# Optimization experiments

Measured on AMD Instinct MI355X. Metric: run time of the kernel, lower is better.

Reference implementation:

```python
import jax, jax.numpy as jnp
import numpy as np

ALPHA = 0.2  # LeakyReLU negative slope


def setup_inputs() -> dict:
    key = jax.random.key(0)
    k1, k2, k3, k4 = jax.random.split(key, 4)
    N, E, F_IN, F_OUT = 100000, 1600000, 128, 32
    x = jax.random.normal(k1, (N, F_IN), dtype=jnp.float32)
    W = jax.random.normal(k2, (F_IN, F_OUT), dtype=jnp.float32) * 0.1
    a = jax.random.normal(k3, (2 * F_OUT, 1), dtype=jnp.float32) * 0.1
    edge_index = jax.random.randint(k4, (2, E), 0, N, dtype=jnp.int64)
    return {"x": x, "W": W, "a": a, "edge_index": edge_index}


def reference(x, W, a, edge_index):
    N = x.shape[0]
    F_OUT = W.shape[1]
    Wx = x @ W  # [N, F_OUT]
    src = edge_index[0]  # row indices (softmax groups)
    dst = edge_index[1]
    # e = leakyrelu([Wx_i || Wx_j] @ a); split a to avoid materializing the concat
    a_src = a[:F_OUT, 0]
    a_dst = a[F_OUT:, 0]
    e = (Wx @ a_src)[src] + (Wx @ a_dst)[dst]  # [E]
    e = jnp.where(e >= 0, e, ALPHA * e)
    # sparse softmax over rows (src)
    m = jax.ops.segment_max(e, src, num_segments=N)  # -inf for empty rows
    m = jnp.where(jnp.isinf(m), 0.0, m)
    exp_v = jnp.exp(e - m[src])
    s = jax.ops.segment_sum(exp_v, src, num_segments=N)
    s = jnp.where(s == 0, 1.0, s)
    att = exp_v / s[src]  # [E]
    # sparse matmul: h[i] = sum_j att[i,j] * Wx[j]
    h = jax.ops.segment_sum(att[:, None] * Wx[dst], src, num_segments=N)
    return jax.nn.elu(h)
```

## Files before the change

### kernel.cpp

```cpp
#include <hip/hip_runtime.h>
#include <hip/hip_bf16.h>
#include <math.h>

#define ALPHA 0.2f
#define F_IN 128
#define F_OUT 32
#define BSHIFT 7
#define BNODES 128
#define DSTBITS 17
#define CHUNK 8192
#define SLABCAP 3072
#define NBKMAX 800
#define MAXPER 6
#define CURSTRIDE 16

typedef __attribute__((ext_vector_type(8))) short short8;
typedef __attribute__((ext_vector_type(4))) float float4v;
typedef __attribute__((ext_vector_type(2))) float float2v;

__device__ __forceinline__ short f2bf(float f) {
    __hip_bfloat16 h = __float2bfloat16(f);
    return __builtin_bit_cast(short, h);
}
__device__ __forceinline__ float bf_lo(unsigned u) {
    return __uint_as_float(u << 16);
}
__device__ __forceinline__ float bf_hi(unsigned u) {
    return __uint_as_float(u & 0xFFFF0000u);
}

__global__ __launch_bounds__(512) void k_phaseA(
    const float* __restrict__ x, const float* __restrict__ W,
    const float* __restrict__ a, unsigned short* __restrict__ Wxh,
    float* __restrict__ s1, float* __restrict__ s2, int nTiles, int N, int nT1,
    const int* __restrict__ src, const int* __restrict__ dst,
    int* __restrict__ bcur, unsigned* __restrict__ packed, int E, int NBK)
{
    if ((int)blockIdx.x < nT1) {
        __shared__ short Wt[32 * 136];
        for (int i = threadIdx.x; i < F_IN * F_OUT; i += 512) {
            int k = i >> 5, n = i & 31;
            Wt[n * 136 + k] = f2bf(W[i]);
        }
        __syncthreads();

        int wave = threadIdx.x >> 6;
        int lane = threadIdx.x & 63;
        int tile = blockIdx.x * 8 + wave;
        if (tile >= nTiles) return;

        int m    = lane & 15;
        int quad = lane >> 4;
        int row  = tile * 16 + m;
        int rowc = row < N ? row : N - 1;

        short8 bf[2][4];
#pragma unroll
        for (int t = 0; t < 2; ++t)
#pragma unroll
            for (int s = 0; s < 4; ++s)
                bf[t][s] = *(const short8*)&Wt[(t * 16 + m) * 136 + s * 32 + quad * 8];

        float4v acc0 = {0.f, 0.f, 0.f, 0.f};
        float4v acc1 = {0.f, 0.f, 0.f, 0.f};
        const float* xr = x + (size_t)rowc * F_IN + quad * 8;
#pragma unroll
        for (int s = 0; s < 4; ++s) {
            float4 xa = *(const float4*)(xr + s * 32);
            float4 xb = *(const float4*)(xr + s * 32 + 4);
            short8 af;
            af[0] = f2bf(xa.x); af[1] = f2bf(xa.y); af[2] = f2bf(xa.z); af[3] = f2bf(xa.w);
            af[4] = f2bf(xb.x); af[5] = f2bf(xb.y); af[6] = f2bf(xb.z); af[7] = f2bf(xb.w);
            acc0 = __builtin_amdgcn_mfma_f32_16x16x32_bf16(af, bf[0][s], acc0, 0, 0, 0);
            acc1 = __builtin_amdgcn_mfma_f32_16x16x32_bf16(af, bf[1][s], acc1, 0, 0, 0);
        }

        int rbase = tile * 16 + quad * 4;
#pragma unroll
        for (int r = 0; r < 4; ++r) {
            if (rbase + r < N) {
                Wxh[(size_t)(rbase + r) * F_OUT + m]      = (unsigned short)f2bf(acc0[r]);
                Wxh[(size_t)(rbase + r) * F_OUT + m + 16] = (unsigned short)f2bf(acc1[r]);
            }
        }

        float a1c0 = a[m], a1c1 = a[m + 16];
        float a2c0 = a[F_OUT + m], a2c1 = a[F_OUT + m + 16];
#pragma unroll
        for (int r = 0; r < 4; ++r) {
            float v1 = acc0[r] * a1c0 + acc1[r] * a1c1;
            float v2 = acc0[r] * a2c0 + acc1[r] * a2c1;
#pragma unroll
            for (int off = 8; off >= 1; off >>= 1) {
                v1 += __shfl_xor(v1, off, 16);
                v2 += __shfl_xor(v2, off, 16);
            }
            if (m == 0 && rbase + r < N) {
                s1[rbase + r] = v1;
                s2[rbase + r] = v2;
            }
        }
    } else {
        __shared__ int hist[NBKMAX];
        __shared__ int cur[NBKMAX];
        int t = threadIdx.x;
        for (int i = t; i < NBK; i += 512) hist[i] = 0;
        __syncthreads();
        int e0 = ((int)blockIdx.x - nT1) * CHUNK;
        int sreg[16], dreg[16];
#pragma unroll
        for (int k = 0; k < 4; ++k) {
            int e = e0 + k * 2048 + t * 4;
            int4 s4, d4;
            if (e + 3 < E) {
                s4 = *(const int4*)&src[e];
                d4 = *(const int4*)&dst[e];
            } else {
                s4.x = (e + 0 < E) ? src[e + 0] : -1;
                s4.y = (e + 1 < E) ? src[e + 1] : -1;
                s4.z = (e + 2 < E) ? src[e + 2] : -1;
                s4.w = (e + 3 < E) ? src[e + 3] : -1;
                d4.x = (e + 0 < E) ? dst[e + 0] : 0;
                d4.y = (e + 1 < E) ? dst[e + 1] : 0;
                d4.z = (e + 2 < E) ? dst[e + 2] : 0;
                d4.w = (e + 3 < E) ? dst[e + 3] : 0;
            }
            sreg[k * 4 + 0] = s4.x; dreg[k * 4 + 0] = d4.x;
            sreg[k * 4 + 1] = s4.y; dreg[k * 4 + 1] = d4.y;
            sreg[k * 4 + 2] = s4.z; dreg[k * 4 + 2] = d4.z;
            sreg[k * 4 + 3] = s4.w; dreg[k * 4 + 3] = d4.w;
        }
#pragma unroll
        for (int k = 0; k < 16; ++k)
            if (sreg[k] >= 0) atomicAdd(&hist[sreg[k] >> BSHIFT], 1);
        __syncthreads();
        for (int i = t; i < NBK; i += 512)
            if (hist[i] > 0) cur[i] = atomicAdd(&bcur[i * CURSTRIDE], hist[i]);
        __syncthreads();
#pragma unroll
        for (int k = 0; k < 16; ++k) {
            if (sreg[k] >= 0) {
                int b = sreg[k] >> BSHIFT;
                int p = atomicAdd(&cur[b], 1);
                if (p < SLABCAP)
                    packed[(size_t)b * SLABCAP + p] =
                        ((unsigned)(sreg[k] & (BNODES - 1)) << DSTBITS) | (unsigned)dreg[k];
            }
        }
    }
}

__global__ __launch_bounds__(512) void k_bnode(
    const unsigned* __restrict__ packed, const int* __restrict__ bcur,
    const float* __restrict__ s1, const float* __restrict__ s2,
    const unsigned short* __restrict__ Wxh, float* __restrict__ out, int N)
{
    __shared__ unsigned sorted[SLABCAP];
    __shared__ int rpl[BNODES];
    __shared__ int degl[BNODES];
    __shared__ int cur[BNODES];
    __shared__ int histl[BNODES];
    __shared__ float s1l[BNODES];
    __shared__ float stageL[8][16][32];
    __shared__ float sumsL[8][16];

    int b = blockIdx.x;
    int t = threadIdx.x;
    int n0 = b << BSHIFT;
    int cnt = min(bcur[b * CURSTRIDE], SLABCAP);
    const unsigned* pb = packed + (size_t)b * SLABCAP;

    if (t < BNODES) {
        histl[t] = 0;
        int n = n0 + t;
        s1l[t] = (n < N) ? s1[n] : 0.f;
    }
    __syncthreads();

    unsigned ereg[MAXPER];
#pragma unroll
    for (int k = 0; k < MAXPER; ++k) {
        int j = k * 512 + t;
        ereg[k] = (j < cnt) ? pb[j] : 0xFFFFFFFFu;
    }
#pragma unroll
    for (int k = 0; k < MAXPER; ++k)
        if (ereg[k] != 0xFFFFFFFFu) atomicAdd(&histl[ereg[k] >> DSTBITS], 1);
    __syncthreads();

    if (t < 64) {
        int aLo = histl[t], aHi = histl[t + 64];
        int sLo = aLo, sHi = aHi;
#pragma unroll
        for (int off = 1; off < 64; off <<= 1) {
            int vLo = __shfl_up(sLo, off, 64);
            int vHi = __shfl_up(sHi, off, 64);
            if (t >= off) { sLo += vLo; sHi += vHi; }
        }
        sHi += __shfl(sLo, 63, 64);
        rpl[t]      = sLo - aLo;  cur[t]      = sLo - aLo;  degl[t]      = aLo;
        rpl[t + 64] = sHi - aHi;  cur[t + 64] = sHi - aHi;  degl[t + 64] = aHi;
    }
    __syncthreads();

#pragma unroll
    for (int k = 0; k < MAXPER; ++k) {
        if (ereg[k] != 0xFFFFFFFFu) {
            int ls = ereg[k] >> DSTBITS;
            int p = atomicAdd(&cur[ls], 1);
            sorted[p] = ereg[k];
        }
    }
    __syncthreads();

    int g   = t >> 4;
    int l4  = t & 15;
    int es  = l4 >> 2;
    int fq  = l4 & 3;
    unsigned fqo = (unsigned)(fq << 4);
    int w    = t >> 6;
    int widx0 = (g & 3) << 2;

    for (int ni = 0; ni < 4; ++ni) {
        int ls = (g << 2) + ni;
        int n = n0 + ls;
        if (n >= N) break;
        int base = rpl[ls];
        int deg  = degl[ls];
        float s1n = s1l[ls];

        float2v acc01 = {0.f, 0.f};
        float2v acc23 = {0.f, 0.f};
        float2v acc45 = {0.f, 0.f};
        float2v acc67 = {0.f, 0.f};
        float sum = 0.f;

        for (int j0 = 0; j0 < deg; j0 += 16) {
            int j = j0 + l4;
            unsigned off_l = 0;
            float p_l = 0.f;
            if (j < deg) {
                int d_l = (int)(sorted[base + j] & ((1u << DSTBITS) - 1));
                off_l = (unsigned)d_l << 6;
                float ev = s1n + s2[d_l];
                ev = fmaxf(ev, ALPHA * ev);
                p_l = __expf(ev);
            }
            sum += p_l;
            int cnt2 = min(16, deg - j0);
            int nIter = (cnt2 + 3) >> 2;
            for (int it = 0; it < nIter; ++it) {
                int e = (it << 2) + es;
                float    p   = __shfl(p_l, e, 16);
                unsigned off = (unsigned)__shfl((int)off_l, e, 16);
                uint4 wv = *(const uint4*)((const char*)Wxh + (off | fqo));
                float2v pp = {p, p};
                acc01 += pp * (float2v){bf_lo(wv.x), bf_hi(wv.x)};
                acc23 += pp * (float2v){bf_lo(wv.y), bf_hi(wv.y)};
                acc45 += pp * (float2v){bf_lo(wv.z), bf_hi(wv.z)};
                acc67 += pp * (float2v){bf_lo(wv.w), bf_hi(wv.w)};
            }
        }
        float a0 = acc01.x, a1 = acc01.y, a2 = acc23.x, a3 = acc23.y;
        float a4 = acc45.x, a5 = acc45.y, a6 = acc67.x, a7 = acc67.y;
#pragma unroll
        for (int off = 4; off <= 8; off <<= 1) {
            a0 += __shfl_xor(a0, off, 16);
            a1 += __shfl_xor(a1, off, 16);
            a2 += __shfl_xor(a2, off, 16);
            a3 += __shfl_xor(a3, off, 16);
            a4 += __shfl_xor(a4, off, 16);
            a5 += __shfl_xor(a5, off, 16);
            a6 += __shfl_xor(a6, off, 16);
            a7 += __shfl_xor(a7, off, 16);
        }
#pragma unroll
        for (int off = 8; off >= 1; off >>= 1)
            sum += __shfl_xor(sum, off, 16);

        if (l4 < 4) {
            float4 v0; v0.x = a0; v0.y = a1; v0.z = a2; v0.w = a3;
            float4 v1; v1.x = a4; v1.y = a5; v1.z = a6; v1.w = a7;
            *(float4*)&stageL[w][widx0 + ni][l4 * 8]     = v0;
            *(float4*)&stageL[w][widx0 + ni][l4 * 8 + 4] = v1;
        }
        if (l4 == 0)
            sumsL[w][widx0 + ni] = sum;
    }

    {
        int lw = t & 63;
        int ln = lw >> 2;
        int fo = (lw & 3) * 8;
        int n = n0 + (w << 4) + ln;
        if (n < N) {
            float s = sumsL[w][ln];
            float inv = (s > 0.f) ? __builtin_amdgcn_rcpf(s) : 0.f;
            const float* sp = &stageL[w][ln][fo];
            float4 h0 = *(const float4*)sp;
            float4 h1 = *(const float4*)(sp + 4);
            h0.x *= inv; h0.y *= inv; h0.z *= inv; h0.w *= inv;
            h1.x *= inv; h1.y *= inv; h1.z *= inv; h1.w *= inv;
            h0.x = h0.x > 0.f ? h0.x : __expf(h0.x) - 1.f;
            h0.y = h0.y > 0.f ? h0.y : __expf(h0.y) - 1.f;
            h0.z = h0.z > 0.f ? h0.z : __expf(h0.z) - 1.f;
            h0.w = h0.w > 0.f ? h0.w : __expf(h0.w) - 1.f;
            h1.x = h1.x > 0.f ? h1.x : __expf(h1.x) - 1.f;
            h1.y = h1.y > 0.f ? h1.y : __expf(h1.y) - 1.f;
            h1.z = h1.z > 0.f ? h1.z : __expf(h1.z) - 1.f;
            h1.w = h1.w > 0.f ? h1.w : __expf(h1.w) - 1.f;
            float* op = &out[(size_t)n * F_OUT + fo];
            *(float4*)op       = h0;
            *(float4*)(op + 4) = h1;
        }
    }
}

extern "C" void kernel_launch(void* const* d_in, const int* in_sizes, int n_in,
                              void* d_out, int out_size, void* d_ws, size_t ws_size,
                              hipStream_t stream)
{
    const float* x = (const float*)d_in[0];
    const float* W = (const float*)d_in[1];
    const float* a = (const float*)d_in[2];
    const int*  ei = (const int*)d_in[3];

    int N = in_sizes[0] / F_IN;
    int E = in_sizes[3] / 2;
    const int* src = ei;
    const int* dst = ei + E;
    int NBK = (N + BNODES - 1) >> BSHIFT;
    int nTiles = (N + 15) / 16;
    int nT1 = (nTiles + 7) / 8;
    int nEB = (E + CHUNK - 1) / CHUNK;

    unsigned short* Wxh = (unsigned short*)d_ws;
    float*    s1       = (float*)d_ws + (size_t)16 * N;
    float*    s2       = s1 + N;
    int*      bcur     = (int*)(s2 + N);
    unsigned* packed   = (unsigned*)(bcur + NBKMAX * CURSTRIDE);

    float* out = (float*)d_out;

    hipMemsetAsync(bcur, 0, (size_t)NBKMAX * CURSTRIDE * 4, stream);

    k_phaseA<<<nT1 + nEB, 512, 0, stream>>>(x, W, a, Wxh, s1, s2, nTiles, N, nT1,
                                            src, dst, bcur, packed, E, NBK);
    k_bnode<<<NBK, 512, 0, stream>>>(packed, bcur, s1, s2, Wxh, out, N);
}
```

Measured before the change: 146.6 us.

## Double edge chunk per block, reload src in scatter pass, rotate bucket reservations

The edge-bucketing blocks now handle 16384 edges each instead of 8192. Instead of holding src/dst in registers, they stream src twice: once for the histogram and once with dst for the scatter. Global bucket-cursor reservations start at a per-block rotated offset to spread atomic contention across buckets. The GEMM branch now issues all x loads before the MFMA loop. These changes halve the number of bucketing blocks and their global atomics, at the cost of re-reading src and holding fewer edges in flight per thread.

```diff
diff --git a/kernel.cpp b/kernel.cpp
--- a/kernel.cpp
+++ b/kernel.cpp
@@ -8,7 +8,7 @@
 #define BSHIFT 7
 #define BNODES 128
 #define DSTBITS 17
-#define CHUNK 8192
+#define CHUNK 16384
 #define SLABCAP 3072
 #define NBKMAX 800
 #define MAXPER 6
@@ -61,16 +61,21 @@
             for (int s = 0; s < 4; ++s)
                 bf[t][s] = *(const short8*)&Wt[(t * 16 + m) * 136 + s * 32 + quad * 8];
 
+        const float* xr = x + (size_t)rowc * F_IN + quad * 8;
+        float4 xa[4], xb[4];
+#pragma unroll
+        for (int s = 0; s < 4; ++s) {
+            xa[s] = *(const float4*)(xr + s * 32);
+            xb[s] = *(const float4*)(xr + s * 32 + 4);
+        }
+
         float4v acc0 = {0.f, 0.f, 0.f, 0.f};
         float4v acc1 = {0.f, 0.f, 0.f, 0.f};
-        const float* xr = x + (size_t)rowc * F_IN + quad * 8;
 #pragma unroll
         for (int s = 0; s < 4; ++s) {
-            float4 xa = *(const float4*)(xr + s * 32);
-            float4 xb = *(const float4*)(xr + s * 32 + 4);
             short8 af;
-            af[0] = f2bf(xa.x); af[1] = f2bf(xa.y); af[2] = f2bf(xa.z); af[3] = f2bf(xa.w);
-            af[4] = f2bf(xb.x); af[5] = f2bf(xb.y); af[6] = f2bf(xb.z); af[7] = f2bf(xb.w);
+            af[0] = f2bf(xa[s].x); af[1] = f2bf(xa[s].y); af[2] = f2bf(xa[s].z); af[3] = f2bf(xa[s].w);
+            af[4] = f2bf(xb[s].x); af[5] = f2bf(xb[s].y); af[6] = f2bf(xb[s].z); af[7] = f2bf(xb[s].w);
             acc0 = __builtin_amdgcn_mfma_f32_16x16x32_bf16(af, bf[0][s], acc0, 0, 0, 0);
             acc1 = __builtin_amdgcn_mfma_f32_16x16x32_bf16(af, bf[1][s], acc1, 0, 0, 0);
         }
@@ -107,9 +112,35 @@
         for (int i = t; i < NBK; i += 512) hist[i] = 0;
         __syncthreads();
         int e0 = ((int)blockIdx.x - nT1) * CHUNK;
-        int sreg[16], dreg[16];
-#pragma unroll
-        for (int k = 0; k < 4; ++k) {
+
+#pragma unroll 2
+        for (int k = 0; k < 8; ++k) {
+            int e = e0 + k * 2048 + t * 4;
+            int4 s4;
+            if (e + 3 < E) {
+                s4 = *(const int4*)&src[e];
+            } else {
+                s4.x = (e + 0 < E) ? src[e + 0] : -1;
+                s4.y = (e + 1 < E) ? src[e + 1] : -1;
+                s4.z = (e + 2 < E) ? src[e + 2] : -1;
+                s4.w = (e + 3 < E) ? src[e + 3] : -1;
+            }
+            if (s4.x >= 0) atomicAdd(&hist[s4.x >> BSHIFT], 1);
+            if (s4.y >= 0) atomicAdd(&hist[s4.y >> BSHIFT], 1);
+            if (s4.z >= 0) atomicAdd(&hist[s4.z >> BSHIFT], 1);
+            if (s4.w >= 0) atomicAdd(&hist[s4.w >> BSHIFT], 1);
+        }
+        __syncthreads();
+
+        int rot = (((int)blockIdx.x - nT1) * 131) % NBK;
+        for (int j = t; j < NBK; j += 512) {
+            int i = j + rot; if (i >= NBK) i -= NBK;
+            if (hist[i] > 0) cur[i] = atomicAdd(&bcur[i * CURSTRIDE], hist[i]);
+        }
+        __syncthreads();
+
+#pragma unroll 2
+        for (int k = 0; k < 8; ++k) {
             int e = e0 + k * 2048 + t * 4;
             int4 s4, d4;
             if (e + 3 < E) {
@@ -125,26 +156,17 @@
                 d4.z = (e + 2 < E) ? dst[e + 2] : 0;
                 d4.w = (e + 3 < E) ? dst[e + 3] : 0;
             }
-            sreg[k * 4 + 0] = s4.x; dreg[k * 4 + 0] = d4.x;
-            sreg[k * 4 + 1] = s4.y; dreg[k * 4 + 1] = d4.y;
-            sreg[k * 4 + 2] = s4.z; dreg[k * 4 + 2] = d4.z;
-            sreg[k * 4 + 3] = s4.w; dreg[k * 4 + 3] = d4.w;
-        }
-#pragma unroll
-        for (int k = 0; k < 16; ++k)
-            if (sreg[k] >= 0) atomicAdd(&hist[sreg[k] >> BSHIFT], 1);
-        __syncthreads();
-        for (int i = t; i < NBK; i += 512)
-            if (hist[i] > 0) cur[i] = atomicAdd(&bcur[i * CURSTRIDE], hist[i]);
-        __syncthreads();
-#pragma unroll
-        for (int k = 0; k < 16; ++k) {
-            if (sreg[k] >= 0) {
-                int b = sreg[k] >> BSHIFT;
-                int p = atomicAdd(&cur[b], 1);
-                if (p < SLABCAP)
-                    packed[(size_t)b * SLABCAP + p] =
-                        ((unsigned)(sreg[k] & (BNODES - 1)) << DSTBITS) | (unsigned)dreg[k];
+            int sreg[4] = {s4.x, s4.y, s4.z, s4.w};
+            int dreg[4] = {d4.x, d4.y, d4.z, d4.w};
+#pragma unroll
+            for (int c = 0; c < 4; ++c) {
+                if (sreg[c] >= 0) {
+                    int b = sreg[c] >> BSHIFT;
+                    int p = atomicAdd(&cur[b], 1);
+                    if (p < SLABCAP)
+                        packed[(size_t)b * SLABCAP + p] =
+                            ((unsigned)(sreg[c] & (BNODES - 1)) << DSTBITS) | (unsigned)dreg[c];
+                }
             }
         }
     }
```

New measurement: 157.0 us. 1.07x slower.

## Store Wx in fp32 instead of bf16 and hoist x loads before MFMA

Applied to the files above, without the earlier changes.

Wx is now kept as fp32 in the workspace rather than bf16, so the gather in the aggregation kernel reads 32 bytes per lane with two float4 loads and skips the bf16 unpacking. This doubles the gathered Wx footprint and the random-gather traffic. It also issues all x row loads ahead of the MFMA loop to overlap their latency. The precision change removes bf16 rounding error on Wx at the cost of extra memory bandwidth.

```diff
diff --git a/kernel.cpp b/kernel.cpp
--- a/kernel.cpp
+++ b/kernel.cpp
@@ -22,16 +22,10 @@
     __hip_bfloat16 h = __float2bfloat16(f);
     return __builtin_bit_cast(short, h);
 }
-__device__ __forceinline__ float bf_lo(unsigned u) {
-    return __uint_as_float(u << 16);
-}
-__device__ __forceinline__ float bf_hi(unsigned u) {
-    return __uint_as_float(u & 0xFFFF0000u);
-}
 
 __global__ __launch_bounds__(512) void k_phaseA(
     const float* __restrict__ x, const float* __restrict__ W,
-    const float* __restrict__ a, unsigned short* __restrict__ Wxh,
+    const float* __restrict__ a, float* __restrict__ Wxh,
     float* __restrict__ s1, float* __restrict__ s2, int nTiles, int N, int nT1,
     const int* __restrict__ src, const int* __restrict__ dst,
     int* __restrict__ bcur, unsigned* __restrict__ packed, int E, int NBK)
@@ -61,16 +55,21 @@
             for (int s = 0; s < 4; ++s)
                 bf[t][s] = *(const short8*)&Wt[(t * 16 + m) * 136 + s * 32 + quad * 8];
 
+        const float* xr = x + (size_t)rowc * F_IN + quad * 8;
+        float4 xa[4], xb[4];
+#pragma unroll
+        for (int s = 0; s < 4; ++s) {
+            xa[s] = *(const float4*)(xr + s * 32);
+            xb[s] = *(const float4*)(xr + s * 32 + 4);
+        }
+
         float4v acc0 = {0.f, 0.f, 0.f, 0.f};
         float4v acc1 = {0.f, 0.f, 0.f, 0.f};
-        const float* xr = x + (size_t)rowc * F_IN + quad * 8;
 #pragma unroll
         for (int s = 0; s < 4; ++s) {
-            float4 xa = *(const float4*)(xr + s * 32);
-            float4 xb = *(const float4*)(xr + s * 32 + 4);
             short8 af;
-            af[0] = f2bf(xa.x); af[1] = f2bf(xa.y); af[2] = f2bf(xa.z); af[3] = f2bf(xa.w);
-            af[4] = f2bf(xb.x); af[5] = f2bf(xb.y); af[6] = f2bf(xb.z); af[7] = f2bf(xb.w);
+            af[0] = f2bf(xa[s].x); af[1] = f2bf(xa[s].y); af[2] = f2bf(xa[s].z); af[3] = f2bf(xa[s].w);
+            af[4] = f2bf(xb[s].x); af[5] = f2bf(xb[s].y); af[6] = f2bf(xb[s].z); af[7] = f2bf(xb[s].w);
             acc0 = __builtin_amdgcn_mfma_f32_16x16x32_bf16(af, bf[0][s], acc0, 0, 0, 0);
             acc1 = __builtin_amdgcn_mfma_f32_16x16x32_bf16(af, bf[1][s], acc1, 0, 0, 0);
         }
@@ -79,8 +78,8 @@
 #pragma unroll
         for (int r = 0; r < 4; ++r) {
             if (rbase + r < N) {
-                Wxh[(size_t)(rbase + r) * F_OUT + m]      = (unsigned short)f2bf(acc0[r]);
-                Wxh[(size_t)(rbase + r) * F_OUT + m + 16] = (unsigned short)f2bf(acc1[r]);
+                Wxh[(size_t)(rbase + r) * F_OUT + m]      = acc0[r];
+                Wxh[(size_t)(rbase + r) * F_OUT + m + 16] = acc1[r];
             }
         }
 
@@ -153,7 +152,7 @@
 __global__ __launch_bounds__(512) void k_bnode(
     const unsigned* __restrict__ packed, const int* __restrict__ bcur,
     const float* __restrict__ s1, const float* __restrict__ s2,
-    const unsigned short* __restrict__ Wxh, float* __restrict__ out, int N)
+    const float* __restrict__ Wxh, float* __restrict__ out, int N)
 {
     __shared__ unsigned sorted[SLABCAP];
     __shared__ int rpl[BNODES];
@@ -217,7 +216,7 @@
     int l4  = t & 15;
     int es  = l4 >> 2;
     int fq  = l4 & 3;
-    unsigned fqo = (unsigned)(fq << 4);
+    unsigned fqo = (unsigned)(fq << 5);
     int w    = t >> 6;
     int widx0 = (g & 3) << 2;
 
@@ -241,7 +240,7 @@
             float p_l = 0.f;
             if (j < deg) {
                 int d_l = (int)(sorted[base + j] & ((1u << DSTBITS) - 1));
-                off_l = (unsigned)d_l << 6;
+                off_l = (unsigned)d_l << 7;
                 float ev = s1n + s2[d_l];
                 ev = fmaxf(ev, ALPHA * ev);
                 p_l = __expf(ev);
@@ -253,12 +252,14 @@
                 int e = (it << 2) + es;
                 float    p   = __shfl(p_l, e, 16);
                 unsigned off = (unsigned)__shfl((int)off_l, e, 16);
-                uint4 wv = *(const uint4*)((const char*)Wxh + (off | fqo));
+                const char* wp = (const char*)Wxh + (off | fqo);
+                float4 w0 = *(const float4*)wp;
+                float4 w1 = *(const float4*)(wp + 16);
                 float2v pp = {p, p};
-                acc01 += pp * (float2v){bf_lo(wv.x), bf_hi(wv.x)};
-                acc23 += pp * (float2v){bf_lo(wv.y), bf_hi(wv.y)};
-                acc45 += pp * (float2v){bf_lo(wv.z), bf_hi(wv.z)};
-                acc67 += pp * (float2v){bf_lo(wv.w), bf_hi(wv.w)};
+                acc01 += pp * (float2v){w0.x, w0.y};
+                acc23 += pp * (float2v){w0.z, w0.w};
+                acc45 += pp * (float2v){w1.x, w1.y};
+                acc67 += pp * (float2v){w1.z, w1.w};
             }
         }
         float a0 = acc01.x, a1 = acc01.y, a2 = acc23.x, a3 = acc23.y;
@@ -334,8 +335,8 @@
     int nT1 = (nTiles + 7) / 8;
     int nEB = (E + CHUNK - 1) / CHUNK;
 
-    unsigned short* Wxh = (unsigned short*)d_ws;
-    float*    s1       = (float*)d_ws + (size_t)16 * N;
+    float*    Wxh      = (float*)d_ws;
+    float*    s1       = (float*)d_ws + (size_t)32 * N;
     float*    s2       = s1 + N;
     int*      bcur     = (int*)(s2 + N);
     unsigned* packed   = (unsigned*)(bcur + NBKMAX * CURSTRIDE);
```

Measured after the change: 152.9 us. 1.04x slower.
